# Kernel optimization log

Hardware: AMD Instinct MI355X
Metric: run time of the kernel (lower is better)

## Reference

```python
import jax, jax.numpy as jnp
import numpy as np

B, T, D = 4, 2048, 1024
H, Dh = 16, 64


def setup_inputs() -> dict:
    key = jax.random.key(0)
    ks = jax.random.split(key, 5)
    # kaiming_normal_ on [H, Dh, D]: fan_in = Dh*D (torch default fan_in over dims[1:]),
    # std = sqrt(2/fan_in); exact init distribution does not affect correctness checks.
    std_qkv = float(np.sqrt(2.0 / (Dh * D)))
    std_o = float(np.sqrt(2.0 / (D * Dh)))
    return {
        "x": jax.random.normal(ks[0], (B, T, D), dtype=jnp.float32),
        "W_Q": jax.random.normal(ks[1], (H, Dh, D), dtype=jnp.float32) * std_qkv,
        "b_Q": jnp.zeros((H, Dh), dtype=jnp.float32),
        "W_K": jax.random.normal(ks[2], (H, Dh, D), dtype=jnp.float32) * std_qkv,
        "b_K": jnp.zeros((H, Dh), dtype=jnp.float32),
        "W_V": jax.random.normal(ks[3], (H, Dh, D), dtype=jnp.float32) * std_qkv,
        "b_V": jnp.zeros((H, Dh), dtype=jnp.float32),
        "W_O": jax.random.normal(ks[4], (H, D, Dh), dtype=jnp.float32) * std_o,
        "b_O": jnp.zeros((D,), dtype=jnp.float32),
    }


def reference(x, W_Q, b_Q, W_K, b_K, W_V, b_V, W_O, b_O):
    # Q/K/V: [batch, tok, heads, d_head]
    Q = jnp.einsum("btd,hkd->bthk", x, W_Q) + b_Q
    K = jnp.einsum("btd,hkd->bthk", x, W_K) + b_K
    V = jnp.einsum("btd,hkd->bthk", x, W_V) + b_V
    d_head = W_Q.shape[1]
    # scores: [batch, heads, tok_Q, tok_K]
    scores = jnp.einsum("bqhk,bshk->bhqs", Q, K) / jnp.sqrt(jnp.asarray(d_head, x.dtype))
    attn = jax.nn.softmax(scores, axis=-1)
    # out per head: [batch, tok_Q, heads, d_head]
    out_h = jnp.einsum("bhqs,bshk->bqhk", attn, V)
    # project back: [batch, tok, d_model]
    return jnp.einsum("bqhk,hdk->bqd", out_h, W_O) + b_O
```

## Files before the change

### kernel.cpp

```cpp
#include <hip/hip_runtime.h>
#include <stdint.h>


typedef __attribute__((ext_vector_type(8))) short bf16x8;
typedef __attribute__((ext_vector_type(4))) short bf16x4;
typedef __attribute__((ext_vector_type(4))) float f32x4;

#define MFMA32 __builtin_amdgcn_mfma_f32_16x16x32_bf16
#define MFMA16 __builtin_amdgcn_mfma_f32_16x16x16bf16_1k

__device__ __forceinline__ unsigned short f2bf(float f) {
  union { float f; unsigned int u; } v; v.f = f;
  unsigned int r = v.u + 0x7FFFu + ((v.u >> 16) & 1u);
  return (unsigned short)(r >> 16);
}

__device__ __forceinline__ void gl_lds16(const void* g, void* l) {
  __builtin_amdgcn_global_load_lds(
      (const __attribute__((address_space(1))) unsigned int*)g,
      (__attribute__((address_space(3))) unsigned int*)l, 16, 0, 0);
}

__device__ __forceinline__ bf16x4 pack_bf4(float a0, float a1, float a2, float a3) {
  union { float f; unsigned u; } x0, x1, x2, x3;
  x0.f = a0; x1.f = a1; x2.f = a2; x3.f = a3;
  unsigned lo = __builtin_amdgcn_perm(x1.u + 0x8000u, x0.u + 0x8000u, 0x07060302u);
  unsigned hi = __builtin_amdgcn_perm(x3.u + 0x8000u, x2.u + 0x8000u, 0x07060302u);
  union { unsigned u[2]; bf16x4 v; } r;
  r.u[0] = lo; r.u[1] = hi;
  return r.v;
}

__global__ __launch_bounds__(256) void conv_bf16(const float* __restrict__ src,
                                                 unsigned short* __restrict__ dst,
                                                 int n8) {
  int i = blockIdx.x * 256 + threadIdx.x;
  if (i >= n8) return;
  const float4* sp = (const float4*)src;
  float4 a = sp[2 * i], b = sp[2 * i + 1];
  union { unsigned short u[8]; uint4 v; } o;
  o.u[0] = f2bf(a.x); o.u[1] = f2bf(a.y); o.u[2] = f2bf(a.z); o.u[3] = f2bf(a.w);
  o.u[4] = f2bf(b.x); o.u[5] = f2bf(b.y); o.u[6] = f2bf(b.z); o.u[7] = f2bf(b.w);
  ((uint4*)dst)[i] = o.v;
}

__global__ __launch_bounds__(256) void transpose_wo(const float* __restrict__ WO,
                                                    unsigned short* __restrict__ Wot) {
  int tid = blockIdx.x * 256 + threadIdx.x;
  int h = tid >> 13, rem = tid & 8191;
  int d = rem >> 3, c = rem & 7;
  const float4* sp = (const float4*)(WO + (size_t)h * 65536 + d * 64 + c * 8);
  float4 a = sp[0], e = sp[1];
  union { unsigned short u[8]; uint4 v; } o;
  o.u[0] = f2bf(a.x); o.u[1] = f2bf(a.y); o.u[2] = f2bf(a.z); o.u[3] = f2bf(a.w);
  o.u[4] = f2bf(e.x); o.u[5] = f2bf(e.y); o.u[6] = f2bf(e.z); o.u[7] = f2bf(e.w);
  *(uint4*)(Wot + (size_t)d * 1024 + h * 64 + c * 8) = o.v;
}

__device__ __forceinline__ void gemm_mainloop_1024(
    const unsigned short* __restrict__ A, const unsigned short* __restrict__ B,
    unsigned short* As, unsigned short* Bs, int m0, int n0, f32x4 acc[4][4]) {
  const int tid = threadIdx.x;
  const int lane = tid & 63, w = tid >> 6;
  const int quad = lane >> 4, l15 = lane & 15;
  const int wm = w & 1, wn = w >> 1;
  int srow[4], scl[4];
#pragma unroll
  for (int u = 0; u < 4; ++u) {
    int s = u * 256 + tid;
    srow[u] = s >> 3;
    scl[u] = ((s & 7) ^ ((s >> 3) & 7)) * 8;
  }
  for (int k0 = 0; k0 < 1024; k0 += 64) {
    __syncthreads();
#pragma unroll
    for (int u = 0; u < 4; ++u) {
      int s = u * 256 + tid;
      gl_lds16(A + (size_t)(m0 + srow[u]) * 1024 + k0 + scl[u], As + s * 8);
      gl_lds16(B + (size_t)(n0 + srow[u]) * 1024 + k0 + scl[u], Bs + s * 8);
    }
    __syncthreads();
    bf16x8 af[4][2], bfr[4][2];
#pragma unroll
    for (int i = 0; i < 4; ++i) {
      int ra = wm * 64 + i * 16 + l15;
      int rb = wn * 64 + i * 16 + l15;
#pragma unroll
      for (int c = 0; c < 2; ++c) {
        af[i][c]  = *(const bf16x8*)(As + ra * 64 + (((c * 4 + quad) ^ (ra & 7)) * 8));
        bfr[i][c] = *(const bf16x8*)(Bs + rb * 64 + (((c * 4 + quad) ^ (rb & 7)) * 8));
      }
    }
#pragma unroll
    for (int mi = 0; mi < 4; ++mi)
#pragma unroll
      for (int nj = 0; nj < 4; ++nj) {
        acc[mi][nj] = MFMA32(af[mi][0], bfr[nj][0], acc[mi][nj], 0, 0, 0);
        acc[mi][nj] = MFMA32(af[mi][1], bfr[nj][1], acc[mi][nj], 0, 0, 0);
      }
  }
}

__global__ __launch_bounds__(256) void gemm_qkv(
    const unsigned short* __restrict__ Xb, const unsigned short* __restrict__ Wqkv,
    const float* __restrict__ bQ, const float* __restrict__ bK,
    const float* __restrict__ bV, unsigned short* __restrict__ Qg,
    unsigned short* __restrict__ Kg, unsigned int* __restrict__ Vpg) {
  __shared__ unsigned short As[128 * 64];
  __shared__ unsigned short Bs[128 * 64];
  const int tid = threadIdx.x, lane = tid & 63, w = tid >> 6;
  const int quad = lane >> 4, l15 = lane & 15;
  const int wm = w & 1, wn = w >> 1;
  const int m0 = blockIdx.x * 128, n0 = blockIdx.y * 128;
  f32x4 acc[4][4];
#pragma unroll
  for (int i = 0; i < 4; ++i)
#pragma unroll
    for (int j = 0; j < 4; ++j) acc[i][j] = (f32x4){0.f, 0.f, 0.f, 0.f};

  gemm_mainloop_1024(Xb, Wqkv, As, Bs, m0, n0, acc);

  const int type = n0 >> 10;
  const int nreg = n0 & 1023;
  const float* bias = (type == 0) ? bQ : (type == 1) ? bK : bV;
#pragma unroll
  for (int nj = 0; nj < 4; ++nj) {
    const int n_loc = nreg + wn * 64 + nj * 16 + l15;
    const int h = n_loc >> 6, kh = n_loc & 63;
    const float bv = bias[n_loc];
#pragma unroll
    for (int mi = 0; mi < 4; ++mi) {
      const int mb = m0 + wm * 64 + mi * 16 + quad * 4;
      const int b = mb >> 11, tb = mb & 2047;
      if (type == 2) {
        uint2 pk;
        pk.x = (unsigned)f2bf(acc[mi][nj][0] + bv) |
               ((unsigned)f2bf(acc[mi][nj][1] + bv) << 16);
        pk.y = (unsigned)f2bf(acc[mi][nj][2] + bv) |
               ((unsigned)f2bf(acc[mi][nj][3] + bv) << 16);
        *(uint2*)(Vpg + ((size_t)(b * 16 + h) * 64 + kh) * 1024 + (tb >> 1)) = pk;
      } else {
        unsigned short* dst =
            ((type == 0) ? Qg : Kg) + ((size_t)(b * 16 + h) * 2048 + tb) * 64 + kh;
        const float sc = (type == 0) ? 0.125f : 1.0f;
        dst[0]   = f2bf((acc[mi][nj][0] + bv) * sc);
        dst[64]  = f2bf((acc[mi][nj][1] + bv) * sc);
        dst[128] = f2bf((acc[mi][nj][2] + bv) * sc);
        dst[192] = f2bf((acc[mi][nj][3] + bv) * sc);
      }
    }
  }
}

__device__ __forceinline__ void stage_kv(const unsigned short* __restrict__ Kb,
                                         const unsigned int* __restrict__ Vb,
                                         unsigned short* smem, int tid, int s0, int b) {
#pragma unroll
  for (int u = 0; u < 2; ++u) {
    int s = u * 256 + tid, row = s >> 3, cl = (s & 7) ^ (row & 7);
    gl_lds16(Kb + (size_t)(s0 + row) * 64 + cl * 8, smem + b * 8192 + s * 8);
    gl_lds16(Vb + (size_t)row * 1024 + (s0 >> 1) + cl * 4,
             smem + b * 8192 + 4096 + s * 8);
  }
}

__global__ __launch_bounds__(256, 4) void flash_attn(
    const unsigned short* __restrict__ Qg, const unsigned short* __restrict__ Kg,
    const unsigned int* __restrict__ Vpg, unsigned short* __restrict__ OH) {
  __shared__ unsigned short smem[16384];
  const int tid = threadIdx.x, lane = tid & 63, w = tid >> 6;
  const int quad = lane >> 4, l15 = lane & 15;
  const int qt = blockIdx.x, bh = blockIdx.y;

  const unsigned short* Qb = Qg + ((size_t)bh * 2048 + qt * 128) * 64;
  const unsigned short* Kb = Kg + (size_t)bh * 2048 * 64;
  const unsigned int*  Vb = Vpg + (size_t)bh * 64 * 1024;

#pragma unroll
  for (int u = 0; u < 4; ++u) {
    int s = u * 256 + tid, row = s >> 3;
    gl_lds16(Qb + row * 64 + ((s & 7) ^ (row & 7)) * 8, smem + s * 8);
  }
  __syncthreads();

  bf16x8 qf[2][2];
#pragma unroll
  for (int qi = 0; qi < 2; ++qi) {
    int row = w * 32 + qi * 16 + l15;
#pragma unroll
    for (int c = 0; c < 2; ++c)
      qf[qi][c] = *(const bf16x8*)(smem + row * 64 + (((c * 4 + quad) ^ (row & 7)) * 8));
  }
  __syncthreads();

  stage_kv(Kb, Vb, smem, tid, 0, 0);

  f32x4 o[2][4];
  float l_part[2] = {0.f, 0.f};
#pragma unroll
  for (int qi = 0; qi < 2; ++qi)
#pragma unroll
    for (int nj = 0; nj < 4; ++nj) o[qi][nj] = (f32x4){0.f, 0.f, 0.f, 0.f};

  for (int t = 0; t < 32; ++t) {
    __syncthreads();
    if (t < 31) stage_kv(Kb, Vb, smem, tid, (t + 1) * 64, (t + 1) & 1);
    const unsigned short* Kd = smem + (t & 1) * 8192;
    const unsigned short* Vd = Kd + 4096;

#pragma unroll
    for (int sj = 0; sj < 4; ++sj) {
      const int krow = sj * 16 + l15;
      bf16x8 ka0 = *(const bf16x8*)(Kd + krow * 64 + ((quad ^ (krow & 7)) * 8));
      bf16x8 ka1 = *(const bf16x8*)(Kd + krow * 64 + (((4 + quad) ^ (krow & 7)) * 8));
      f32x4 S0 = (f32x4){0.f, 0.f, 0.f, 0.f}, S1 = S0;
      S0 = MFMA32(ka0, qf[0][0], S0, 0, 0, 0);
      S0 = MFMA32(ka1, qf[0][1], S0, 0, 0, 0);
      S1 = MFMA32(ka0, qf[1][0], S1, 0, 0, 0);
      S1 = MFMA32(ka1, qf[1][1], S1, 0, 0, 0);

      float e00 = __expf(S0[0]), e01 = __expf(S0[1]);
      float e02 = __expf(S0[2]), e03 = __expf(S0[3]);
      float e10 = __expf(S1[0]), e11 = __expf(S1[1]);
      float e12 = __expf(S1[2]), e13 = __expf(S1[3]);
      l_part[0] += (e00 + e01) + (e02 + e03);
      l_part[1] += (e10 + e11) + (e12 + e13);
      bf16x4 pa0 = pack_bf4(e00, e01, e02, e03);
      bf16x4 pa1 = pack_bf4(e10, e11, e12, e13);

#pragma unroll
      for (int nj = 0; nj < 4; ++nj) {
        const int vrow = nj * 16 + l15;
        const int j = (2 * sj + (quad >> 1)) ^ (vrow & 7);
        bf16x4 vbf = *(const bf16x4*)(Vd + vrow * 64 + j * 8 + (quad & 1) * 4);
        o[0][nj] = MFMA16(pa0, vbf, o[0][nj], 0, 0, 0);
        o[1][nj] = MFMA16(pa1, vbf, o[1][nj], 0, 0, 0);
      }
    }
  }

  const int b = bh >> 4, h = bh & 15;
#pragma unroll
  for (int qi = 0; qi < 2; ++qi) {
    float l = l_part[qi];
    l += __shfl_xor(l, 16);
    l += __shfl_xor(l, 32);
    float linv = 1.0f / l;
#pragma unroll
    for (int r = 0; r < 4; ++r) {
      float lr = __shfl(linv, 4 * quad + r);
      int trow = qt * 128 + w * 32 + qi * 16 + 4 * quad + r;
#pragma unroll
      for (int nj = 0; nj < 4; ++nj) {
        int col = h * 64 + nj * 16 + l15;
        OH[((size_t)b * 2048 + trow) * 1024 + col] = f2bf(o[qi][nj][r] * lr);
      }
    }
  }
}

__global__ __launch_bounds__(256) void gemm_o(
    const unsigned short* __restrict__ OHm, const unsigned short* __restrict__ Wot,
    const float* __restrict__ bO, float* __restrict__ Out) {
  __shared__ unsigned short As[128 * 64];
  __shared__ unsigned short Bs[128 * 64];
  const int tid = threadIdx.x, lane = tid & 63, w = tid >> 6;
  const int quad = lane >> 4, l15 = lane & 15;
  const int wm = w & 1, wn = w >> 1;
  const int m0 = blockIdx.x * 128, n0 = blockIdx.y * 128;
  f32x4 acc[4][4];
#pragma unroll
  for (int i = 0; i < 4; ++i)
#pragma unroll
    for (int j = 0; j < 4; ++j) acc[i][j] = (f32x4){0.f, 0.f, 0.f, 0.f};

  gemm_mainloop_1024(OHm, Wot, As, Bs, m0, n0, acc);

#pragma unroll
  for (int nj = 0; nj < 4; ++nj) {
    const int n = n0 + wn * 64 + nj * 16 + l15;
    const float bv = bO[n];
#pragma unroll
    for (int mi = 0; mi < 4; ++mi) {
      const int mb = m0 + wm * 64 + mi * 16 + quad * 4;
#pragma unroll
      for (int r = 0; r < 4; ++r)
        Out[(size_t)(mb + r) * 1024 + n] = acc[mi][nj][r] + bv;
    }
  }
}

extern "C" void kernel_launch(void* const* d_in, const int* in_sizes, int n_in,
                              void* d_out, int out_size, void* d_ws, size_t ws_size,
                              hipStream_t stream) {
  const float* x  = (const float*)d_in[0];
  const float* WQ = (const float*)d_in[1];
  const float* bQ = (const float*)d_in[2];
  const float* WK = (const float*)d_in[3];
  const float* bK = (const float*)d_in[4];
  const float* WV = (const float*)d_in[5];
  const float* bV = (const float*)d_in[6];
  const float* WO = (const float*)d_in[7];
  const float* bO = (const float*)d_in[8];
  float* out = (float*)d_out;

  char* ws = (char*)d_ws;
  unsigned short* Xb   = (unsigned short*)(ws);
  unsigned short* OH   = (unsigned short*)(ws);
  unsigned short* Wqkv = (unsigned short*)(ws + 16777216);
  unsigned short* Wot  = (unsigned short*)(ws + 23068672);
  unsigned short* Qg   = (unsigned short*)(ws + 25165824);
  unsigned short* Kg   = (unsigned short*)(ws + 41943040);
  unsigned int*   Vpg  = (unsigned int*)  (ws + 58720256);

  conv_bf16<<<4096, 256, 0, stream>>>(x, Xb, 1048576);
  conv_bf16<<<512, 256, 0, stream>>>(WQ, Wqkv, 131072);
  conv_bf16<<<512, 256, 0, stream>>>(WK, Wqkv + 1048576, 131072);
  conv_bf16<<<512, 256, 0, stream>>>(WV, Wqkv + 2097152, 131072);
  transpose_wo<<<512, 256, 0, stream>>>(WO, Wot);

  dim3 g1(64, 24);
  gemm_qkv<<<g1, 256, 0, stream>>>(Xb, Wqkv, bQ, bK, bV, Qg, Kg, Vpg);
  dim3 g2(16, 64);
  flash_attn<<<g2, 256, 0, stream>>>(Qg, Kg, Vpg, OH);
  dim3 g3(64, 8);
  gemm_o<<<g3, 256, 0, stream>>>(OH, Wot, bO, out);
}
```

Before: 305.2 us.

## Merge prep kernels, use exp2 with folded log2e, and widen PV MFMA to k32

Five conversion and transpose launches become one prep_all kernel to cut launch overhead. The Q scale now folds in log2(e), so the softmax uses the hardware exp2 directly instead of __expf. The attention inner loop is restructured to use 16x16x32 MFMAs for P·V with a permuted K-row ordering and a new LDS swizzle (rho), halving the number of PV MFMA instructions and using wider V loads. Packing P to bf16 now truncates rather than rounds, which slightly changes numerics.

```diff
diff --git a/kernel.cpp b/kernel.cpp
--- a/kernel.cpp
+++ b/kernel.cpp
@@ -3,11 +3,15 @@
 
 
 typedef __attribute__((ext_vector_type(8))) short bf16x8;
-typedef __attribute__((ext_vector_type(4))) short bf16x4;
 typedef __attribute__((ext_vector_type(4))) float f32x4;
 
 #define MFMA32 __builtin_amdgcn_mfma_f32_16x16x32_bf16
-#define MFMA16 __builtin_amdgcn_mfma_f32_16x16x16bf16_1k
+
+#if __has_builtin(__builtin_amdgcn_exp2f)
+#define EXP2(x) __builtin_amdgcn_exp2f(x)
+#else
+#define EXP2(x) exp2f(x)
+#endif
 
 __device__ __forceinline__ unsigned short f2bf(float f) {
   union { float f; unsigned int u; } v; v.f = f;
@@ -21,21 +25,15 @@
       (__attribute__((address_space(3))) unsigned int*)l, 16, 0, 0);
 }
 
-__device__ __forceinline__ bf16x4 pack_bf4(float a0, float a1, float a2, float a3) {
-  union { float f; unsigned u; } x0, x1, x2, x3;
-  x0.f = a0; x1.f = a1; x2.f = a2; x3.f = a3;
-  unsigned lo = __builtin_amdgcn_perm(x1.u + 0x8000u, x0.u + 0x8000u, 0x07060302u);
-  unsigned hi = __builtin_amdgcn_perm(x3.u + 0x8000u, x2.u + 0x8000u, 0x07060302u);
-  union { unsigned u[2]; bf16x4 v; } r;
-  r.u[0] = lo; r.u[1] = hi;
-  return r.v;
-}
-
-__global__ __launch_bounds__(256) void conv_bf16(const float* __restrict__ src,
-                                                 unsigned short* __restrict__ dst,
-                                                 int n8) {
-  int i = blockIdx.x * 256 + threadIdx.x;
-  if (i >= n8) return;
+__device__ __forceinline__ unsigned packbf2(float lo, float hi) {
+  union { float f; unsigned u; } a, b; a.f = lo; b.f = hi;
+  return __builtin_amdgcn_perm(b.u, a.u, 0x07060302u);
+}
+
+__device__ __forceinline__ int rho(int r) { return (r & 3) | ((r >> 1) & 4); }
+
+__device__ __forceinline__ void conv8(const float* __restrict__ src,
+                                      unsigned short* __restrict__ dst, int i) {
   const float4* sp = (const float4*)src;
   float4 a = sp[2 * i], b = sp[2 * i + 1];
   union { unsigned short u[8]; uint4 v; } o;
@@ -44,17 +42,31 @@
   ((uint4*)dst)[i] = o.v;
 }
 
-__global__ __launch_bounds__(256) void transpose_wo(const float* __restrict__ WO,
-                                                    unsigned short* __restrict__ Wot) {
-  int tid = blockIdx.x * 256 + threadIdx.x;
-  int h = tid >> 13, rem = tid & 8191;
-  int d = rem >> 3, c = rem & 7;
-  const float4* sp = (const float4*)(WO + (size_t)h * 65536 + d * 64 + c * 8);
-  float4 a = sp[0], e = sp[1];
-  union { unsigned short u[8]; uint4 v; } o;
-  o.u[0] = f2bf(a.x); o.u[1] = f2bf(a.y); o.u[2] = f2bf(a.z); o.u[3] = f2bf(a.w);
-  o.u[4] = f2bf(e.x); o.u[5] = f2bf(e.y); o.u[6] = f2bf(e.z); o.u[7] = f2bf(e.w);
-  *(uint4*)(Wot + (size_t)d * 1024 + h * 64 + c * 8) = o.v;
+__global__ __launch_bounds__(256) void prep_all(
+    const float* __restrict__ x, const float* __restrict__ WQ,
+    const float* __restrict__ WK, const float* __restrict__ WV,
+    const float* __restrict__ WO, unsigned short* __restrict__ Xb,
+    unsigned short* __restrict__ Wqkv, unsigned short* __restrict__ Wot) {
+  const int bx = blockIdx.x, t = threadIdx.x;
+  if (bx < 4096) {
+    conv8(x, Xb, bx * 256 + t);
+  } else if (bx < 4608) {
+    conv8(WQ, Wqkv, (bx - 4096) * 256 + t);
+  } else if (bx < 5120) {
+    conv8(WK, Wqkv + 1048576, (bx - 4608) * 256 + t);
+  } else if (bx < 5632) {
+    conv8(WV, Wqkv + 2097152, (bx - 5120) * 256 + t);
+  } else {
+    int tid = (bx - 5632) * 256 + t;
+    int h = tid >> 13, rem = tid & 8191;
+    int d = rem >> 3, c = rem & 7;
+    const float4* sp = (const float4*)(WO + (size_t)h * 65536 + d * 64 + c * 8);
+    float4 a = sp[0], e = sp[1];
+    union { unsigned short u[8]; uint4 v; } o;
+    o.u[0] = f2bf(a.x); o.u[1] = f2bf(a.y); o.u[2] = f2bf(a.z); o.u[3] = f2bf(a.w);
+    o.u[4] = f2bf(e.x); o.u[5] = f2bf(e.y); o.u[6] = f2bf(e.z); o.u[7] = f2bf(e.w);
+    *(uint4*)(Wot + (size_t)d * 1024 + h * 64 + c * 8) = o.v;
+  }
 }
 
 __device__ __forceinline__ void gemm_mainloop_1024(
@@ -142,7 +154,7 @@
       } else {
         unsigned short* dst =
             ((type == 0) ? Qg : Kg) + ((size_t)(b * 16 + h) * 2048 + tb) * 64 + kh;
-        const float sc = (type == 0) ? 0.125f : 1.0f;
+        const float sc = (type == 0) ? 0.18033688011112042f : 1.0f;
         dst[0]   = f2bf((acc[mi][nj][0] + bv) * sc);
         dst[64]  = f2bf((acc[mi][nj][1] + bv) * sc);
         dst[128] = f2bf((acc[mi][nj][2] + bv) * sc);
@@ -157,9 +169,9 @@
                                          unsigned short* smem, int tid, int s0, int b) {
 #pragma unroll
   for (int u = 0; u < 2; ++u) {
-    int s = u * 256 + tid, row = s >> 3, cl = (s & 7) ^ (row & 7);
-    gl_lds16(Kb + (size_t)(s0 + row) * 64 + cl * 8, smem + b * 8192 + s * 8);
-    gl_lds16(Vb + (size_t)row * 1024 + (s0 >> 1) + cl * 4,
+    int s = u * 256 + tid, row = s >> 3, g = (s & 7) ^ rho(row);
+    gl_lds16(Kb + (size_t)(s0 + row) * 64 + g * 8, smem + b * 8192 + s * 8);
+    gl_lds16(Vb + (size_t)row * 1024 + (s0 >> 1) + g * 4,
              smem + b * 8192 + 4096 + s * 8);
   }
 }
@@ -209,32 +221,36 @@
     const unsigned short* Vd = Kd + 4096;
 
 #pragma unroll
-    for (int sj = 0; sj < 4; ++sj) {
-      const int krow = sj * 16 + l15;
-      bf16x8 ka0 = *(const bf16x8*)(Kd + krow * 64 + ((quad ^ (krow & 7)) * 8));
-      bf16x8 ka1 = *(const bf16x8*)(Kd + krow * 64 + (((4 + quad) ^ (krow & 7)) * 8));
-      f32x4 S0 = (f32x4){0.f, 0.f, 0.f, 0.f}, S1 = S0;
-      S0 = MFMA32(ka0, qf[0][0], S0, 0, 0, 0);
-      S0 = MFMA32(ka1, qf[0][1], S0, 0, 0, 0);
-      S1 = MFMA32(ka0, qf[1][0], S1, 0, 0, 0);
-      S1 = MFMA32(ka1, qf[1][1], S1, 0, 0, 0);
-
-      float e00 = __expf(S0[0]), e01 = __expf(S0[1]);
-      float e02 = __expf(S0[2]), e03 = __expf(S0[3]);
-      float e10 = __expf(S1[0]), e11 = __expf(S1[1]);
-      float e12 = __expf(S1[2]), e13 = __expf(S1[3]);
-      l_part[0] += (e00 + e01) + (e02 + e03);
-      l_part[1] += (e10 + e11) + (e12 + e13);
-      bf16x4 pa0 = pack_bf4(e00, e01, e02, e03);
-      bf16x4 pa1 = pack_bf4(e10, e11, e12, e13);
-
+    for (int blk = 0; blk < 2; ++blk) {
+      bf16x8 vb[4];
 #pragma unroll
       for (int nj = 0; nj < 4; ++nj) {
-        const int vrow = nj * 16 + l15;
-        const int j = (2 * sj + (quad >> 1)) ^ (vrow & 7);
-        bf16x4 vbf = *(const bf16x4*)(Vd + vrow * 64 + j * 8 + (quad & 1) * 4);
-        o[0][nj] = MFMA16(pa0, vbf, o[0][nj], 0, 0, 0);
-        o[1][nj] = MFMA16(pa1, vbf, o[1][nj], 0, 0, 0);
+        int vrow = nj * 16 + l15;
+        vb[nj] = *(const bf16x8*)(Vd + vrow * 64 + (((blk * 4 + quad) ^ rho(vrow)) * 8));
+      }
+      union { unsigned u[4]; bf16x8 v; } pa0, pa1;
+#pragma unroll
+      for (int v = 0; v < 2; ++v) {
+        int krow = blk * 32 + 8 * (l15 >> 2) + 4 * v + (l15 & 3);
+        const unsigned short* kr = Kd + krow * 64;
+        bf16x8 ka0 = *(const bf16x8*)(kr + ((quad ^ rho(krow)) * 8));
+        bf16x8 ka1 = *(const bf16x8*)(kr + (((4 + quad) ^ rho(krow)) * 8));
+        f32x4 S0 = (f32x4){0.f, 0.f, 0.f, 0.f}, S1 = S0;
+        S0 = MFMA32(ka0, qf[0][0], S0, 0, 0, 0);
+        S0 = MFMA32(ka1, qf[0][1], S0, 0, 0, 0);
+        S1 = MFMA32(ka0, qf[1][0], S1, 0, 0, 0);
+        S1 = MFMA32(ka1, qf[1][1], S1, 0, 0, 0);
+        float e0 = EXP2(S0[0]), e1 = EXP2(S0[1]), e2 = EXP2(S0[2]), e3 = EXP2(S0[3]);
+        float f0 = EXP2(S1[0]), f1 = EXP2(S1[1]), f2 = EXP2(S1[2]), f3 = EXP2(S1[3]);
+        l_part[0] += (e0 + e1) + (e2 + e3);
+        l_part[1] += (f0 + f1) + (f2 + f3);
+        pa0.u[2 * v] = packbf2(e0, e1); pa0.u[2 * v + 1] = packbf2(e2, e3);
+        pa1.u[2 * v] = packbf2(f0, f1); pa1.u[2 * v + 1] = packbf2(f2, f3);
+      }
+#pragma unroll
+      for (int nj = 0; nj < 4; ++nj) {
+        o[0][nj] = MFMA32(pa0.v, vb[nj], o[0][nj], 0, 0, 0);
+        o[1][nj] = MFMA32(pa1.v, vb[nj], o[1][nj], 0, 0, 0);
       }
     }
   }
@@ -313,11 +329,7 @@
   unsigned short* Kg   = (unsigned short*)(ws + 41943040);
   unsigned int*   Vpg  = (unsigned int*)  (ws + 58720256);
 
-  conv_bf16<<<4096, 256, 0, stream>>>(x, Xb, 1048576);
-  conv_bf16<<<512, 256, 0, stream>>>(WQ, Wqkv, 131072);
-  conv_bf16<<<512, 256, 0, stream>>>(WK, Wqkv + 1048576, 131072);
-  conv_bf16<<<512, 256, 0, stream>>>(WV, Wqkv + 2097152, 131072);
-  transpose_wo<<<512, 256, 0, stream>>>(WO, Wot);
+  prep_all<<<6144, 256, 0, stream>>>(x, WQ, WK, WV, WO, Xb, Wqkv, Wot);
 
   dim3 g1(64, 24);
   gemm_qkv<<<g1, 256, 0, stream>>>(Xb, Wqkv, bQ, bK, bV, Qg, Kg, Vpg);
```

Result: faster. 288.9 us (-5.3%).
